# Optimization experiments

Measured on AMD Instinct MI355X. Metric: run time of the kernel, lower is better.

Reference implementation:

```python
import jax, jax.numpy as jnp
import numpy as np

NH = 16  # num_attention_heads
DH = 64  # attention_head_size
HID = NH * DH
TYPE_VOCAB = 2


def setup_inputs() -> dict:
    key = jax.random.key(0)
    ks = jax.random.split(key, 10)
    B, S = 4, 2048
    s = 0.02
    return {
        "hidden_states": jax.random.normal(ks[0], (B, S, HID), jnp.float32),
        "attention_mask": jnp.zeros((B, 1, 1, S), jnp.float32),
        "seg_ids": jax.random.randint(ks[1], (B, S), 0, TYPE_VOCAB),
        "Wq": jax.random.normal(ks[2], (HID, HID), jnp.float32) * s,
        "bq": jnp.zeros((HID,), jnp.float32),
        "Wk": jax.random.normal(ks[3], (HID, HID), jnp.float32) * s,  # key has NO bias (F.linear with weight only)
        "Wv": jax.random.normal(ks[4], (HID, HID), jnp.float32) * s,
        "bv": jnp.zeros((HID,), jnp.float32),
        "seg_table": jax.random.normal(ks[5], (TYPE_VOCAB, HID), jnp.float32) * s,
        "b_q_s": jnp.zeros((1, NH, 1, DH), jnp.float32),
    }


def reference(hidden_states, attention_mask, seg_ids, Wq, bq, Wk, Wv, bv, seg_table, b_q_s):
    B, S, H = hidden_states.shape
    # QKV projections (key projection has no bias, matching F.linear(x, key.weight))
    q = hidden_states @ Wq.T + bq
    k = hidden_states @ Wk.T
    v = hidden_states @ Wv.T + bv
    # [B, NH, S, DH]
    q = q.reshape(B, S, NH, DH).transpose(0, 2, 1, 3)
    k = k.reshape(B, S, NH, DH).transpose(0, 2, 1, 3)
    v = v.reshape(B, S, NH, DH).transpose(0, 2, 1, 3)
    scale = 1.0 / np.sqrt(DH).astype(np.float32)
    scores = jnp.einsum('bhid,bhjd->bhij', q * scale, k)
    # segment-embedding bias: seg_rep [B, S, NH, DH]
    seg_rep = seg_table[seg_ids].reshape(B, S, NH, DH)
    qs = jnp.einsum('bhid,bjhd->bhij', q + b_q_s, seg_rep)
    scores = scores + qs + attention_mask
    probs = jax.nn.softmax(scores, axis=-1)  # dropout: eval mode (identity)
    ctx = jnp.einsum('bhij,bhjd->bihd', probs, v).reshape(B, S, H)
    return ctx
```

## Files before the change

### kernel.cpp

```cpp
#include <hip/hip_runtime.h>
#include <cstdint>
#include <cmath>

#define RLN2 1.44269504088896340736f

typedef __attribute__((ext_vector_type(8))) short short8;
typedef __attribute__((ext_vector_type(4))) short short4v;
typedef __attribute__((ext_vector_type(4))) float f32x4;
typedef __attribute__((ext_vector_type(16))) float f32x16;
typedef __attribute__((ext_vector_type(4))) unsigned int uint4v;

__device__ __forceinline__ unsigned short f2bf(float f) {
  unsigned int u = __float_as_uint(f);
  u += 0x7fffu + ((u >> 16) & 1u);
  return (unsigned short)(u >> 16);
}

__device__ __forceinline__ unsigned int cvt_pk_bf16(float lo, float hi) {
  unsigned int r;
  asm("v_cvt_pk_bf16_f32 %0, %1, %2" : "=v"(r) : "v"(lo), "v"(hi));
  return r;
}

__device__ __forceinline__ float fast_exp2(float x) {
#if __has_builtin(__builtin_amdgcn_exp2f)
  return __builtin_amdgcn_exp2f(x);
#else
  return exp2f(x);
#endif
}

__device__ __forceinline__ void gload16(const void* g, void* l) {
  __builtin_amdgcn_global_load_lds(
      (const __attribute__((address_space(1))) unsigned int*)g,
      (__attribute__((address_space(3))) unsigned int*)l,
      16, 0, 0);
}


__global__ void __launch_bounds__(256) k_cvt_hs(const float* __restrict__ src,
                                                unsigned short* __restrict__ dst) {
  size_t i = (size_t)blockIdx.x * 256 + threadIdx.x;
  const float4* s = (const float4*)src + i * 2;
  float4 a = s[0], b = s[1];
  short8 o;
  o[0] = (short)f2bf(a.x); o[1] = (short)f2bf(a.y); o[2] = (short)f2bf(a.z); o[3] = (short)f2bf(a.w);
  o[4] = (short)f2bf(b.x); o[5] = (short)f2bf(b.y); o[6] = (short)f2bf(b.z); o[7] = (short)f2bf(b.w);
  ((short8*)dst)[i] = o;
}

__global__ void __launch_bounds__(256) k_cvt_w(const float* __restrict__ Wq,
                                               const float* __restrict__ Wk,
                                               const float* __restrict__ Wv,
                                               unsigned short* __restrict__ dst) {
  size_t i = (size_t)blockIdx.x * 256 + threadIdx.x;
  int e = (int)(i * 8);
  int n = e >> 10, c = e & 1023;
  const float* row = (n < 1024) ? (Wq + (size_t)n * 1024)
                   : (n < 2048) ? (Wk + (size_t)(n - 1024) * 1024)
                                : (Wv + (size_t)(n - 2048) * 1024);
  const float4* s = (const float4*)(row + c);
  float4 a = s[0], b = s[1];
  short8 o;
  o[0] = (short)f2bf(a.x); o[1] = (short)f2bf(a.y); o[2] = (short)f2bf(a.z); o[3] = (short)f2bf(a.w);
  o[4] = (short)f2bf(b.x); o[5] = (short)f2bf(b.y); o[6] = (short)f2bf(b.z); o[7] = (short)f2bf(b.w);
  ((short8*)dst)[i] = o;
}

__global__ void __launch_bounds__(256) k_seg(const int* __restrict__ seg_ids,
                                             const float* __restrict__ seg_table,
                                             const float* __restrict__ mask,
                                             unsigned short* __restrict__ Kaug,
                                             float* __restrict__ mask2) {
  size_t i = (size_t)blockIdx.x * 256 + threadIdx.x;
  int e = (int)(i * 8);
  int jl = e >> 10;
  int r  = e & 1023;
  if (r == 0) mask2[jl] = mask[jl] * RLN2;
  int sid = seg_ids[jl];
  const float4* s = (const float4*)(seg_table + (size_t)sid * 1024 + r);
  float4 a = s[0], b = s[1];
  short8 o;
  o[0] = (short)f2bf(a.x); o[1] = (short)f2bf(a.y); o[2] = (short)f2bf(a.z); o[3] = (short)f2bf(a.w);
  o[4] = (short)f2bf(b.x); o[5] = (short)f2bf(b.y); o[6] = (short)f2bf(b.z); o[7] = (short)f2bf(b.w);
  int b_ = jl >> 11, j = jl & 2047;
  int h = r >> 6, d = r & 63;
  size_t off = ((size_t)(b_ * 16 + h) * 2048 + j) * 128 + 64 + d;
  *(short8*)(Kaug + off) = o;
}

__global__ void __launch_bounds__(256) k_gemm(const unsigned short* __restrict__ A,
                                              const unsigned short* __restrict__ Bw,
                                              const float* __restrict__ bq,
                                              const float* __restrict__ bv,
                                              const float* __restrict__ bqs,
                                              unsigned short* __restrict__ Qaug,
                                              unsigned short* __restrict__ Kaug,
                                              unsigned short* __restrict__ Vt) {
  __shared__ unsigned short As[128 * 32];
  __shared__ unsigned short Bs[128 * 32];
  int n0 = blockIdx.x * 128;
  int m0 = blockIdx.y * 128;
  int tid = threadIdx.x;
  int w = tid >> 6, lane = tid & 63;
  int wr = (w >> 1) * 64, wc = (w & 1) * 64;
  int rA = lane & 15;
  int kg = (lane >> 4) * 16;
  f32x4 acc[4][4] = {};
  const char* Ab = (const char*)A;
  const char* Bb = (const char*)Bw;

  for (int kt = 0; kt < 32; ++kt) {
    int kb0 = kt * 64;
#pragma unroll
    for (int c = 0; c < 2; ++c) {
      int chunk = w * 2 + c;
      int y = chunk * 1024 + lane * 16;
      int row = y >> 6, colb = y & 63;
      gload16(Ab + (size_t)(m0 + row) * 2048 + kb0 + colb, (char*)As + chunk * 1024);
      gload16(Bb + (size_t)(n0 + row) * 2048 + kb0 + colb, (char*)Bs + chunk * 1024);
    }
    __syncthreads();
    short8 af[4], bfr[4];
#pragma unroll
    for (int m = 0; m < 4; ++m)
      af[m] = *(const short8*)((const char*)As + (wr + m * 16 + rA) * 64 + kg);
#pragma unroll
    for (int n = 0; n < 4; ++n)
      bfr[n] = *(const short8*)((const char*)Bs + (wc + n * 16 + rA) * 64 + kg);
#pragma unroll
    for (int m = 0; m < 4; ++m)
#pragma unroll
      for (int n = 0; n < 4; ++n)
        acc[m][n] = __builtin_amdgcn_mfma_f32_16x16x32_bf16(af[m], bfr[n], acc[m][n], 0, 0, 0);
    __syncthreads();
  }

  int seg = n0 >> 10;
  int colbase = n0 & 1023;
  int g = lane >> 4;
#pragma unroll
  for (int n = 0; n < 4; ++n) {
    int o = colbase + wc + n * 16 + (lane & 15);
    int h = o >> 6, d = o & 63;
    float bias = 0.f, bqsv = 0.f;
    if (seg == 0) { bias = bq[o]; bqsv = bqs[o]; }
    else if (seg == 2) { bias = bv[o]; }
#pragma unroll
    for (int m = 0; m < 4; ++m) {
      if (seg == 2) {
        int i = m0 + wr + m * 16 + g * 4;
        int b_ = i >> 11, sdx = i & 2047;
        int bh = b_ * 16 + h;
        int pos = (sdx & ~63) + 32 * ((m >> 1) & 1) + 16 * (m & 1) + 8 * (g & 1) + 4 * ((g >> 1) & 1);
        short4v pv;
#pragma unroll
        for (int r = 0; r < 4; ++r)
          pv[r] = (short)f2bf(acc[m][n][r] + bias);
        *(short4v*)(Vt + (size_t)bh * 131072 + (size_t)d * 2048 + pos) = pv;
      } else {
#pragma unroll
        for (int r = 0; r < 4; ++r) {
          int i = m0 + wr + m * 16 + g * 4 + r;
          int b_ = i >> 11, sdx = i & 2047;
          float val = acc[m][n][r];
          size_t tok = (size_t)(b_ * 16 + h) * 2048 + sdx;
          if (seg == 0) {
            float qv = val + bias;
            Qaug[tok * 128 + d]      = f2bf(qv * (0.125f * RLN2));
            Qaug[tok * 128 + 64 + d] = f2bf((qv + bqsv) * RLN2);
          } else {
            Kaug[tok * 128 + d] = f2bf(val);
          }
        }
      }
    }
  }
}

__global__ void __launch_bounds__(512, 4) k_attn(const unsigned short* __restrict__ Qaug,
                                                 const unsigned short* __restrict__ Kaug,
                                                 const unsigned short* __restrict__ Vt,
                                                 const float* __restrict__ mask2,
                                                 float* __restrict__ out) {
  __shared__ char smem[49152];
  char* Ksb = smem;
  char* Vsb = smem + 32768;

  int qt = blockIdx.x, h = blockIdx.y, b_ = blockIdx.z;
  int bh = b_ * 16 + h;
  int i0 = qt * 256;
  int tid = threadIdx.x, w = tid >> 6, lane = tid & 63;
  int q = lane & 31, hi = lane >> 5;
  int swzq = (q & 7) << 4;
  const char* Qg = (const char*)Qaug + (size_t)bh * 2048 * 256;
  const char* Kg = (const char*)Kaug + (size_t)bh * 2048 * 256;
  const char* Vg = (const char*)Vt + (size_t)bh * 64 * 4096;
  const float* maskb = mask2 + (size_t)b_ * 2048;

  int foff[8];
#pragma unroll
  for (int ds = 0; ds < 8; ++ds)
    foff[ds] = (ds * 32 + hi * 16) ^ swzq;

  int kst_row = lane >> 4, kst_x = (lane & 15) * 16;
  int vst_dv = lane >> 3;
  int vst_x = ((lane & 7) * 16) ^ ((vst_dv & 7) << 4);

#pragma unroll
  for (int c = 0; c < 2; ++c) {
    int ck = w * 2 + c;
    int krow = ck * 4 + kst_row;
    gload16(Kg + (size_t)krow * 256 + (kst_x ^ ((krow & 7) << 4)), Ksb + ck * 1024);
  }
  {
    int dv = w * 8 + vst_dv;
    gload16(Vg + (size_t)dv * 4096 + vst_x, Vsb + w * 1024);
  }

  short8 qf[8];
  {
    const char* qrow = Qg + (size_t)(i0 + w * 32 + q) * 256 + hi * 16;
#pragma unroll
    for (int ds = 0; ds < 8; ++ds)
      qf[ds] = *(const short8*)(qrow + ds * 32);
  }
  __syncthreads();

  float m_run = -1e30f, l_run = 0.f;
  f32x16 accO[2] = {};

  for (int t = 0; t < 32; ++t) {
    int cur = t & 1, nxt = cur ^ 1;
    int j0 = t * 64;
    if (t < 31) {
      int jn = j0 + 64;
      char* kd = Ksb + nxt * 16384;
      char* vd = Vsb + nxt * 8192;
#pragma unroll
      for (int c = 0; c < 2; ++c) {
        int ck = w * 2 + c;
        int krow = ck * 4 + kst_row;
        gload16(Kg + (size_t)(jn + krow) * 256 + (kst_x ^ ((krow & 7) << 4)), kd + ck * 1024);
      }
      {
        int dv = w * 8 + vst_dv;
        gload16(Vg + (size_t)dv * 4096 + jn * 2 + vst_x, vd + w * 1024);
      }
    }
    const char* kq = Ksb + cur * 16384 + q * 256;
    const char* vq = Vsb + cur * 8192 + q * 128;

    f32x16 s0 = {}, s1 = {};
    __builtin_amdgcn_s_setprio(1);
#pragma unroll
    for (int ds = 0; ds < 8; ++ds) {
      short8 kf0 = *(const short8*)(kq + foff[ds]);
      short8 kf1 = *(const short8*)(kq + foff[ds] + 8192);
      s0 = __builtin_amdgcn_mfma_f32_32x32x16_bf16(kf0, qf[ds], s0, 0, 0, 0);
      s1 = __builtin_amdgcn_mfma_f32_32x32x16_bf16(kf1, qf[ds], s1, 0, 0, 0);
    }
    __builtin_amdgcn_s_setprio(0);

#pragma unroll
    for (int c = 0; c < 4; ++c) {
      f32x4 mv0 = *(const f32x4*)(maskb + j0 + 8 * c + 4 * hi);
      f32x4 mv1 = *(const f32x4*)(maskb + j0 + 32 + 8 * c + 4 * hi);
#pragma unroll
      for (int r = 0; r < 4; ++r) {
        s0[4 * c + r] += mv0[r];
        s1[4 * c + r] += mv1[r];
      }
    }

    {
      f32x16 mx;
#pragma unroll
      for (int i = 0; i < 16; ++i) mx[i] = fmaxf(s0[i], s1[i]);
#pragma unroll
      for (int i = 0; i < 8; ++i) mx[i] = fmaxf(mx[i], mx[i + 8]);
#pragma unroll
      for (int i = 0; i < 4; ++i) mx[i] = fmaxf(mx[i], mx[i + 4]);
      float tm = fmaxf(fmaxf(mx[0], mx[1]), fmaxf(mx[2], mx[3]));
      tm = fmaxf(tm, __shfl_xor(tm, 32));

      if (__any(tm > m_run + 8.0f)) {
        float mn = fmaxf(m_run, tm);
        float alpha = fast_exp2(m_run - mn);
        m_run = mn;
        l_run *= alpha;
#pragma unroll
        for (int i = 0; i < 16; ++i) { accO[0][i] *= alpha; accO[1][i] *= alpha; }
      }
    }
    {
      f32x16 es;
#pragma unroll
      for (int i = 0; i < 16; ++i) {
        float e0 = fast_exp2(s0[i] - m_run);
        float e1 = fast_exp2(s1[i] - m_run);
        s0[i] = e0; s1[i] = e1;
        es[i] = e0 + e1;
      }
#pragma unroll
      for (int i = 0; i < 8; ++i) es[i] += es[i + 8];
#pragma unroll
      for (int i = 0; i < 4; ++i) es[i] += es[i + 4];
      float ps = (es[0] + es[1]) + (es[2] + es[3]);
      ps += __shfl_xor(ps, 32);
      l_run += ps;
    }

    uint4v pk[4];
#pragma unroll
    for (int ks = 0; ks < 4; ++ks) {
      int o = 8 * (ks & 1);
      const f32x16& sv = (ks < 2) ? s0 : s1;
      pk[ks][0] = cvt_pk_bf16(sv[o + 0], sv[o + 1]);
      pk[ks][1] = cvt_pk_bf16(sv[o + 2], sv[o + 3]);
      pk[ks][2] = cvt_pk_bf16(sv[o + 4], sv[o + 5]);
      pk[ks][3] = cvt_pk_bf16(sv[o + 6], sv[o + 7]);
    }

    __builtin_amdgcn_s_setprio(1);
#pragma unroll
    for (int ks = 0; ks < 4; ++ks) {
      short8 pf = __builtin_bit_cast(short8, pk[ks]);
      short8 vf0 = *(const short8*)(vq + foff[ks]);
      short8 vf1 = *(const short8*)(vq + foff[ks] + 4096);
      accO[0] = __builtin_amdgcn_mfma_f32_32x32x16_bf16(vf0, pf, accO[0], 0, 0, 0);
      accO[1] = __builtin_amdgcn_mfma_f32_32x32x16_bf16(vf1, pf, accO[1], 0, 0, 0);
    }
    __builtin_amdgcn_s_setprio(0);
    __syncthreads();
  }

  float inv = 1.0f / l_run;
  float* orow = out + ((size_t)b_ * 2048 + i0 + w * 32 + q) * 1024 + h * 64;
#pragma unroll
  for (int vh = 0; vh < 2; ++vh) {
#pragma unroll
    for (int c = 0; c < 4; ++c) {
      f32x4 o;
      o[0] = accO[vh][4 * c + 0] * inv;
      o[1] = accO[vh][4 * c + 1] * inv;
      o[2] = accO[vh][4 * c + 2] * inv;
      o[3] = accO[vh][4 * c + 3] * inv;
      *(f32x4*)(orow + vh * 32 + 8 * c + 4 * hi) = o;
    }
  }
}

extern "C" void kernel_launch(void* const* d_in, const int* in_sizes, int n_in,
                              void* d_out, int out_size, void* d_ws, size_t ws_size,
                              hipStream_t stream) {
  (void)in_sizes; (void)n_in; (void)out_size; (void)ws_size;
  const float* hs        = (const float*)d_in[0];
  const float* mask      = (const float*)d_in[1];
  const int*   seg_ids   = (const int*)d_in[2];
  const float* Wq        = (const float*)d_in[3];
  const float* bq        = (const float*)d_in[4];
  const float* Wk        = (const float*)d_in[5];
  const float* Wv        = (const float*)d_in[6];
  const float* bv        = (const float*)d_in[7];
  const float* seg_table = (const float*)d_in[8];
  const float* bqs       = (const float*)d_in[9];
  float* out = (float*)d_out;
  char* ws = (char*)d_ws;

  unsigned short* hsb  = (unsigned short*)(ws + 0);
  unsigned short* Wcat = (unsigned short*)(ws + 16777216);
  unsigned short* Qaug = (unsigned short*)(ws + 23068672);
  unsigned short* Kaug = (unsigned short*)(ws + 56623104);
  unsigned short* Vt   = (unsigned short*)(ws + 90177536);
  float*          mask2 = (float*)(ws + 0);

  k_cvt_hs<<<dim3(4096), dim3(256), 0, stream>>>(hs, hsb);
  k_cvt_w<<<dim3(1536), dim3(256), 0, stream>>>(Wq, Wk, Wv, Wcat);
  k_gemm<<<dim3(24, 64), dim3(256), 0, stream>>>(hsb, Wcat, bq, bv, bqs, Qaug, Kaug, Vt);
  k_seg<<<dim3(4096), dim3(256), 0, stream>>>(seg_ids, seg_table, mask, Kaug, mask2);
  k_attn<<<dim3(8, 16, 4), dim3(512), 0, stream>>>(Qaug, Kaug, Vt, mask2, out);
}
```

Before: 267.8 us.

## Split KV tile into two 32-key halves for softmax/MFMA overlap

The 64-key inner tile is now processed as two 32-key halves, each with its own online-softmax update followed by its PV MFMAs. The QK MFMAs for the second half can overlap the softmax of the first half, and the mask loads are hoisted ahead of the MFMAs. In exchange, the max/rescale check and the rescale of accO run twice per tile, and the QK MFMA chains become serial dependency chains of 8 instead of two interleaved chains.

```diff
diff --git a/kernel.cpp b/kernel.cpp
--- a/kernel.cpp
+++ b/kernel.cpp
@@ -251,39 +251,40 @@
     const char* kq = Ksb + cur * 16384 + q * 256;
     const char* vq = Vsb + cur * 8192 + q * 128;
 
+    f32x4 mv0[4], mv1[4];
+#pragma unroll
+    for (int c = 0; c < 4; ++c) {
+      mv0[c] = *(const f32x4*)(maskb + j0 + 8 * c + 4 * hi);
+      mv1[c] = *(const f32x4*)(maskb + j0 + 32 + 8 * c + 4 * hi);
+    }
+
     f32x16 s0 = {}, s1 = {};
     __builtin_amdgcn_s_setprio(1);
 #pragma unroll
     for (int ds = 0; ds < 8; ++ds) {
       short8 kf0 = *(const short8*)(kq + foff[ds]);
+      s0 = __builtin_amdgcn_mfma_f32_32x32x16_bf16(kf0, qf[ds], s0, 0, 0, 0);
+    }
+#pragma unroll
+    for (int ds = 0; ds < 8; ++ds) {
       short8 kf1 = *(const short8*)(kq + foff[ds] + 8192);
-      s0 = __builtin_amdgcn_mfma_f32_32x32x16_bf16(kf0, qf[ds], s0, 0, 0, 0);
       s1 = __builtin_amdgcn_mfma_f32_32x32x16_bf16(kf1, qf[ds], s1, 0, 0, 0);
     }
     __builtin_amdgcn_s_setprio(0);
 
-#pragma unroll
-    for (int c = 0; c < 4; ++c) {
-      f32x4 mv0 = *(const f32x4*)(maskb + j0 + 8 * c + 4 * hi);
-      f32x4 mv1 = *(const f32x4*)(maskb + j0 + 32 + 8 * c + 4 * hi);
-#pragma unroll
-      for (int r = 0; r < 4; ++r) {
-        s0[4 * c + r] += mv0[r];
-        s1[4 * c + r] += mv1[r];
-      }
-    }
-
+    uint4v pkA[2];
     {
-      f32x16 mx;
-#pragma unroll
-      for (int i = 0; i < 16; ++i) mx[i] = fmaxf(s0[i], s1[i]);
-#pragma unroll
-      for (int i = 0; i < 8; ++i) mx[i] = fmaxf(mx[i], mx[i + 8]);
-#pragma unroll
-      for (int i = 0; i < 4; ++i) mx[i] = fmaxf(mx[i], mx[i + 4]);
+#pragma unroll
+      for (int c = 0; c < 4; ++c)
+#pragma unroll
+        for (int r = 0; r < 4; ++r)
+          s0[4 * c + r] += mv0[c][r];
+      f32x4 mx;
+#pragma unroll
+      for (int i = 0; i < 4; ++i)
+        mx[i] = fmaxf(fmaxf(s0[i], s0[i + 4]), fmaxf(s0[i + 8], s0[i + 12]));
       float tm = fmaxf(fmaxf(mx[0], mx[1]), fmaxf(mx[2], mx[3]));
       tm = fmaxf(tm, __shfl_xor(tm, 32));
-
       if (__any(tm > m_run + 8.0f)) {
         float mn = fmaxf(m_run, tm);
         float alpha = fast_exp2(m_run - mn);
@@ -292,16 +293,9 @@
 #pragma unroll
         for (int i = 0; i < 16; ++i) { accO[0][i] *= alpha; accO[1][i] *= alpha; }
       }
-    }
-    {
       f32x16 es;
 #pragma unroll
-      for (int i = 0; i < 16; ++i) {
-        float e0 = fast_exp2(s0[i] - m_run);
-        float e1 = fast_exp2(s1[i] - m_run);
-        s0[i] = e0; s1[i] = e1;
-        es[i] = e0 + e1;
-      }
+      for (int i = 0; i < 16; ++i) { es[i] = fast_exp2(s0[i] - m_run); s0[i] = es[i]; }
 #pragma unroll
       for (int i = 0; i < 8; ++i) es[i] += es[i + 8];
 #pragma unroll
@@ -309,25 +303,74 @@
       float ps = (es[0] + es[1]) + (es[2] + es[3]);
       ps += __shfl_xor(ps, 32);
       l_run += ps;
-    }
-
-    uint4v pk[4];
-#pragma unroll
-    for (int ks = 0; ks < 4; ++ks) {
-      int o = 8 * (ks & 1);
-      const f32x16& sv = (ks < 2) ? s0 : s1;
-      pk[ks][0] = cvt_pk_bf16(sv[o + 0], sv[o + 1]);
-      pk[ks][1] = cvt_pk_bf16(sv[o + 2], sv[o + 3]);
-      pk[ks][2] = cvt_pk_bf16(sv[o + 4], sv[o + 5]);
-      pk[ks][3] = cvt_pk_bf16(sv[o + 6], sv[o + 7]);
+      pkA[0][0] = cvt_pk_bf16(s0[0], s0[1]);
+      pkA[0][1] = cvt_pk_bf16(s0[2], s0[3]);
+      pkA[0][2] = cvt_pk_bf16(s0[4], s0[5]);
+      pkA[0][3] = cvt_pk_bf16(s0[6], s0[7]);
+      pkA[1][0] = cvt_pk_bf16(s0[8], s0[9]);
+      pkA[1][1] = cvt_pk_bf16(s0[10], s0[11]);
+      pkA[1][2] = cvt_pk_bf16(s0[12], s0[13]);
+      pkA[1][3] = cvt_pk_bf16(s0[14], s0[15]);
     }
 
     __builtin_amdgcn_s_setprio(1);
 #pragma unroll
-    for (int ks = 0; ks < 4; ++ks) {
-      short8 pf = __builtin_bit_cast(short8, pk[ks]);
+    for (int ks = 0; ks < 2; ++ks) {
+      short8 pf = __builtin_bit_cast(short8, pkA[ks]);
       short8 vf0 = *(const short8*)(vq + foff[ks]);
       short8 vf1 = *(const short8*)(vq + foff[ks] + 4096);
+      accO[0] = __builtin_amdgcn_mfma_f32_32x32x16_bf16(vf0, pf, accO[0], 0, 0, 0);
+      accO[1] = __builtin_amdgcn_mfma_f32_32x32x16_bf16(vf1, pf, accO[1], 0, 0, 0);
+    }
+    __builtin_amdgcn_s_setprio(0);
+
+    uint4v pkB[2];
+    {
+#pragma unroll
+      for (int c = 0; c < 4; ++c)
+#pragma unroll
+        for (int r = 0; r < 4; ++r)
+          s1[4 * c + r] += mv1[c][r];
+      f32x4 mx;
+#pragma unroll
+      for (int i = 0; i < 4; ++i)
+        mx[i] = fmaxf(fmaxf(s1[i], s1[i + 4]), fmaxf(s1[i + 8], s1[i + 12]));
+      float tm = fmaxf(fmaxf(mx[0], mx[1]), fmaxf(mx[2], mx[3]));
+      tm = fmaxf(tm, __shfl_xor(tm, 32));
+      if (__any(tm > m_run + 8.0f)) {
+        float mn = fmaxf(m_run, tm);
+        float alpha = fast_exp2(m_run - mn);
+        m_run = mn;
+        l_run *= alpha;
+#pragma unroll
+        for (int i = 0; i < 16; ++i) { accO[0][i] *= alpha; accO[1][i] *= alpha; }
+      }
+      f32x16 es;
+#pragma unroll
+      for (int i = 0; i < 16; ++i) { es[i] = fast_exp2(s1[i] - m_run); s1[i] = es[i]; }
+#pragma unroll
+      for (int i = 0; i < 8; ++i) es[i] += es[i + 8];
+#pragma unroll
+      for (int i = 0; i < 4; ++i) es[i] += es[i + 4];
+      float ps = (es[0] + es[1]) + (es[2] + es[3]);
+      ps += __shfl_xor(ps, 32);
+      l_run += ps;
+      pkB[0][0] = cvt_pk_bf16(s1[0], s1[1]);
+      pkB[0][1] = cvt_pk_bf16(s1[2], s1[3]);
+      pkB[0][2] = cvt_pk_bf16(s1[4], s1[5]);
+      pkB[0][3] = cvt_pk_bf16(s1[6], s1[7]);
+      pkB[1][0] = cvt_pk_bf16(s1[8], s1[9]);
+      pkB[1][1] = cvt_pk_bf16(s1[10], s1[11]);
+      pkB[1][2] = cvt_pk_bf16(s1[12], s1[13]);
+      pkB[1][3] = cvt_pk_bf16(s1[14], s1[15]);
+    }
+
+    __builtin_amdgcn_s_setprio(1);
+#pragma unroll
+    for (int ks = 0; ks < 2; ++ks) {
+      short8 pf = __builtin_bit_cast(short8, pkB[ks]);
+      short8 vf0 = *(const short8*)(vq + foff[ks + 2]);
+      short8 vf1 = *(const short8*)(vq + foff[ks + 2] + 4096);
       accO[0] = __builtin_amdgcn_mfma_f32_32x32x16_bf16(vf0, pf, accO[0], 0, 0, 0);
       accO[1] = __builtin_amdgcn_mfma_f32_32x32x16_bf16(vf1, pf, accO[1], 0, 0, 0);
     }
```

Result: slower. 962.2 us (+259.4%).

## Fuse prep kernels into one launch and vectorize Q/K GEMM epilogue stores

Applied to the files above, without the earlier changes.

Merges the three conversion and segment-embedding kernels into a single k_prep launch and drops the mask2 buffer, folding the log2(e) mask scaling into an fma inside the attention kernel. For Q and K tiles the GEMM swaps its MFMA operands so each lane holds four consecutive output columns. This lets the epilogue write packed 8-byte bf16 stores through v_cvt_pk_bf16 instead of scattered 2-byte stores. The aim is to cut launch overhead and uncoalesced epilogue writes, at the cost of a seg-dependent branch in the MFMA loop.

```diff
diff --git a/kernel.cpp b/kernel.cpp
--- a/kernel.cpp
+++ b/kernel.cpp
@@ -9,6 +9,7 @@
 typedef __attribute__((ext_vector_type(4))) float f32x4;
 typedef __attribute__((ext_vector_type(16))) float f32x16;
 typedef __attribute__((ext_vector_type(4))) unsigned int uint4v;
+typedef __attribute__((ext_vector_type(2))) unsigned int uint2v;
 
 __device__ __forceinline__ unsigned short f2bf(float f) {
   unsigned int u = __float_as_uint(f);
@@ -37,56 +38,53 @@
       16, 0, 0);
 }
 
-
-__global__ void __launch_bounds__(256) k_cvt_hs(const float* __restrict__ src,
-                                                unsigned short* __restrict__ dst) {
-  size_t i = (size_t)blockIdx.x * 256 + threadIdx.x;
-  const float4* s = (const float4*)src + i * 2;
-  float4 a = s[0], b = s[1];
-  short8 o;
-  o[0] = (short)f2bf(a.x); o[1] = (short)f2bf(a.y); o[2] = (short)f2bf(a.z); o[3] = (short)f2bf(a.w);
-  o[4] = (short)f2bf(b.x); o[5] = (short)f2bf(b.y); o[6] = (short)f2bf(b.z); o[7] = (short)f2bf(b.w);
-  ((short8*)dst)[i] = o;
-}
-
-__global__ void __launch_bounds__(256) k_cvt_w(const float* __restrict__ Wq,
-                                               const float* __restrict__ Wk,
-                                               const float* __restrict__ Wv,
-                                               unsigned short* __restrict__ dst) {
-  size_t i = (size_t)blockIdx.x * 256 + threadIdx.x;
-  int e = (int)(i * 8);
-  int n = e >> 10, c = e & 1023;
-  const float* row = (n < 1024) ? (Wq + (size_t)n * 1024)
-                   : (n < 2048) ? (Wk + (size_t)(n - 1024) * 1024)
-                                : (Wv + (size_t)(n - 2048) * 1024);
-  const float4* s = (const float4*)(row + c);
-  float4 a = s[0], b = s[1];
-  short8 o;
-  o[0] = (short)f2bf(a.x); o[1] = (short)f2bf(a.y); o[2] = (short)f2bf(a.z); o[3] = (short)f2bf(a.w);
-  o[4] = (short)f2bf(b.x); o[5] = (short)f2bf(b.y); o[6] = (short)f2bf(b.z); o[7] = (short)f2bf(b.w);
-  ((short8*)dst)[i] = o;
-}
-
-__global__ void __launch_bounds__(256) k_seg(const int* __restrict__ seg_ids,
-                                             const float* __restrict__ seg_table,
-                                             const float* __restrict__ mask,
-                                             unsigned short* __restrict__ Kaug,
-                                             float* __restrict__ mask2) {
-  size_t i = (size_t)blockIdx.x * 256 + threadIdx.x;
-  int e = (int)(i * 8);
-  int jl = e >> 10;
-  int r  = e & 1023;
-  if (r == 0) mask2[jl] = mask[jl] * RLN2;
-  int sid = seg_ids[jl];
-  const float4* s = (const float4*)(seg_table + (size_t)sid * 1024 + r);
-  float4 a = s[0], b = s[1];
-  short8 o;
-  o[0] = (short)f2bf(a.x); o[1] = (short)f2bf(a.y); o[2] = (short)f2bf(a.z); o[3] = (short)f2bf(a.w);
-  o[4] = (short)f2bf(b.x); o[5] = (short)f2bf(b.y); o[6] = (short)f2bf(b.z); o[7] = (short)f2bf(b.w);
-  int b_ = jl >> 11, j = jl & 2047;
-  int h = r >> 6, d = r & 63;
-  size_t off = ((size_t)(b_ * 16 + h) * 2048 + j) * 128 + 64 + d;
-  *(short8*)(Kaug + off) = o;
+__global__ void __launch_bounds__(256) k_prep(const float* __restrict__ hs,
+                                              const float* __restrict__ Wq,
+                                              const float* __restrict__ Wk,
+                                              const float* __restrict__ Wv,
+                                              const int* __restrict__ seg_ids,
+                                              const float* __restrict__ seg_table,
+                                              unsigned short* __restrict__ hsb,
+                                              unsigned short* __restrict__ Wcat,
+                                              unsigned short* __restrict__ Kaug) {
+  int blk = blockIdx.x;
+  if (blk < 4096) {
+    size_t i = (size_t)blk * 256 + threadIdx.x;
+    const float4* s = (const float4*)hs + i * 2;
+    float4 a = s[0], b = s[1];
+    short8 o;
+    o[0] = (short)f2bf(a.x); o[1] = (short)f2bf(a.y); o[2] = (short)f2bf(a.z); o[3] = (short)f2bf(a.w);
+    o[4] = (short)f2bf(b.x); o[5] = (short)f2bf(b.y); o[6] = (short)f2bf(b.z); o[7] = (short)f2bf(b.w);
+    ((short8*)hsb)[i] = o;
+  } else if (blk < 5632) {
+    size_t i = (size_t)(blk - 4096) * 256 + threadIdx.x;
+    int e = (int)(i * 8);
+    int n = e >> 10, c = e & 1023;
+    const float* row = (n < 1024) ? (Wq + (size_t)n * 1024)
+                     : (n < 2048) ? (Wk + (size_t)(n - 1024) * 1024)
+                                  : (Wv + (size_t)(n - 2048) * 1024);
+    const float4* s = (const float4*)(row + c);
+    float4 a = s[0], b = s[1];
+    short8 o;
+    o[0] = (short)f2bf(a.x); o[1] = (short)f2bf(a.y); o[2] = (short)f2bf(a.z); o[3] = (short)f2bf(a.w);
+    o[4] = (short)f2bf(b.x); o[5] = (short)f2bf(b.y); o[6] = (short)f2bf(b.z); o[7] = (short)f2bf(b.w);
+    ((short8*)Wcat)[i] = o;
+  } else {
+    size_t i = (size_t)(blk - 5632) * 256 + threadIdx.x;
+    int e = (int)(i * 8);
+    int jl = e >> 10;
+    int r  = e & 1023;
+    int sid = seg_ids[jl];
+    const float4* s = (const float4*)(seg_table + (size_t)sid * 1024 + r);
+    float4 a = s[0], b = s[1];
+    short8 o;
+    o[0] = (short)f2bf(a.x); o[1] = (short)f2bf(a.y); o[2] = (short)f2bf(a.z); o[3] = (short)f2bf(a.w);
+    o[4] = (short)f2bf(b.x); o[5] = (short)f2bf(b.y); o[6] = (short)f2bf(b.z); o[7] = (short)f2bf(b.w);
+    int b_ = jl >> 11, j = jl & 2047;
+    int h = r >> 6, d = r & 63;
+    size_t off = ((size_t)(b_ * 16 + h) * 2048 + j) * 128 + 64 + d;
+    *(short8*)(Kaug + off) = o;
+  }
 }
 
 __global__ void __launch_bounds__(256) k_gemm(const unsigned short* __restrict__ A,
@@ -106,6 +104,7 @@
   int wr = (w >> 1) * 64, wc = (w & 1) * 64;
   int rA = lane & 15;
   int kg = (lane >> 4) * 16;
+  int seg = n0 >> 10;
   f32x4 acc[4][4] = {};
   const char* Ab = (const char*)A;
   const char* Bb = (const char*)Bw;
@@ -128,27 +127,32 @@
 #pragma unroll
     for (int n = 0; n < 4; ++n)
       bfr[n] = *(const short8*)((const char*)Bs + (wc + n * 16 + rA) * 64 + kg);
-#pragma unroll
-    for (int m = 0; m < 4; ++m)
-#pragma unroll
-      for (int n = 0; n < 4; ++n)
-        acc[m][n] = __builtin_amdgcn_mfma_f32_16x16x32_bf16(af[m], bfr[n], acc[m][n], 0, 0, 0);
+    if (seg == 2) {
+#pragma unroll
+      for (int m = 0; m < 4; ++m)
+#pragma unroll
+        for (int n = 0; n < 4; ++n)
+          acc[m][n] = __builtin_amdgcn_mfma_f32_16x16x32_bf16(af[m], bfr[n], acc[m][n], 0, 0, 0);
+    } else {
+#pragma unroll
+      for (int m = 0; m < 4; ++m)
+#pragma unroll
+        for (int n = 0; n < 4; ++n)
+          acc[m][n] = __builtin_amdgcn_mfma_f32_16x16x32_bf16(bfr[n], af[m], acc[m][n], 0, 0, 0);
+    }
     __syncthreads();
   }
 
-  int seg = n0 >> 10;
   int colbase = n0 & 1023;
   int g = lane >> 4;
-#pragma unroll
-  for (int n = 0; n < 4; ++n) {
-    int o = colbase + wc + n * 16 + (lane & 15);
-    int h = o >> 6, d = o & 63;
-    float bias = 0.f, bqsv = 0.f;
-    if (seg == 0) { bias = bq[o]; bqsv = bqs[o]; }
-    else if (seg == 2) { bias = bv[o]; }
-#pragma unroll
-    for (int m = 0; m < 4; ++m) {
-      if (seg == 2) {
+  if (seg == 2) {
+#pragma unroll
+    for (int n = 0; n < 4; ++n) {
+      int o = colbase + wc + n * 16 + (lane & 15);
+      int h = o >> 6, d = o & 63;
+      float bias = bv[o];
+#pragma unroll
+      for (int m = 0; m < 4; ++m) {
         int i = m0 + wr + m * 16 + g * 4;
         int b_ = i >> 11, sdx = i & 2047;
         int bh = b_ * 16 + h;
@@ -158,20 +162,38 @@
         for (int r = 0; r < 4; ++r)
           pv[r] = (short)f2bf(acc[m][n][r] + bias);
         *(short4v*)(Vt + (size_t)bh * 131072 + (size_t)d * 2048 + pos) = pv;
-      } else {
-#pragma unroll
-        for (int r = 0; r < 4; ++r) {
-          int i = m0 + wr + m * 16 + g * 4 + r;
-          int b_ = i >> 11, sdx = i & 2047;
-          float val = acc[m][n][r];
-          size_t tok = (size_t)(b_ * 16 + h) * 2048 + sdx;
-          if (seg == 0) {
-            float qv = val + bias;
-            Qaug[tok * 128 + d]      = f2bf(qv * (0.125f * RLN2));
-            Qaug[tok * 128 + 64 + d] = f2bf((qv + bqsv) * RLN2);
-          } else {
-            Kaug[tok * 128 + d] = f2bf(val);
-          }
+      }
+    }
+  } else {
+    int tok16 = lane & 15, g4 = g * 4;
+#pragma unroll
+    for (int m = 0; m < 4; ++m) {
+      int i = m0 + wr + m * 16 + tok16;
+      int b_ = i >> 11, sdx = i & 2047;
+#pragma unroll
+      for (int n = 0; n < 4; ++n) {
+        int o0 = colbase + wc + n * 16 + g4;
+        int h = o0 >> 6, d0 = o0 & 63;
+        size_t tok = (size_t)(b_ * 16 + h) * 2048 + sdx;
+        if (seg == 0) {
+          f32x4 bqv = *(const f32x4*)(bq + o0);
+          f32x4 bqs4 = *(const f32x4*)(bqs + o0);
+          float qv0 = acc[m][n][0] + bqv[0], qv1 = acc[m][n][1] + bqv[1];
+          float qv2 = acc[m][n][2] + bqv[2], qv3 = acc[m][n][3] + bqv[3];
+          const float sc = 0.125f * RLN2;
+          uint2v p1;
+          p1[0] = cvt_pk_bf16(qv0 * sc, qv1 * sc);
+          p1[1] = cvt_pk_bf16(qv2 * sc, qv3 * sc);
+          *(uint2v*)(Qaug + tok * 128 + d0) = p1;
+          uint2v p2;
+          p2[0] = cvt_pk_bf16((qv0 + bqs4[0]) * RLN2, (qv1 + bqs4[1]) * RLN2);
+          p2[1] = cvt_pk_bf16((qv2 + bqs4[2]) * RLN2, (qv3 + bqs4[3]) * RLN2);
+          *(uint2v*)(Qaug + tok * 128 + 64 + d0) = p2;
+        } else {
+          uint2v p1;
+          p1[0] = cvt_pk_bf16(acc[m][n][0], acc[m][n][1]);
+          p1[1] = cvt_pk_bf16(acc[m][n][2], acc[m][n][3]);
+          *(uint2v*)(Kaug + tok * 128 + d0) = p1;
         }
       }
     }
@@ -181,7 +203,7 @@
 __global__ void __launch_bounds__(512, 4) k_attn(const unsigned short* __restrict__ Qaug,
                                                  const unsigned short* __restrict__ Kaug,
                                                  const unsigned short* __restrict__ Vt,
-                                                 const float* __restrict__ mask2,
+                                                 const float* __restrict__ mask,
                                                  float* __restrict__ out) {
   __shared__ char smem[49152];
   char* Ksb = smem;
@@ -196,7 +218,7 @@
   const char* Qg = (const char*)Qaug + (size_t)bh * 2048 * 256;
   const char* Kg = (const char*)Kaug + (size_t)bh * 2048 * 256;
   const char* Vg = (const char*)Vt + (size_t)bh * 64 * 4096;
-  const float* maskb = mask2 + (size_t)b_ * 2048;
+  const float* maskb = mask + (size_t)b_ * 2048;
 
   int foff[8];
 #pragma unroll
@@ -268,8 +290,8 @@
       f32x4 mv1 = *(const f32x4*)(maskb + j0 + 32 + 8 * c + 4 * hi);
 #pragma unroll
       for (int r = 0; r < 4; ++r) {
-        s0[4 * c + r] += mv0[r];
-        s1[4 * c + r] += mv1[r];
+        s0[4 * c + r] = fmaf(mv0[r], RLN2, s0[4 * c + r]);
+        s1[4 * c + r] = fmaf(mv1[r], RLN2, s1[4 * c + r]);
       }
     }
 
@@ -373,11 +395,9 @@
   unsigned short* Qaug = (unsigned short*)(ws + 23068672);
   unsigned short* Kaug = (unsigned short*)(ws + 56623104);
   unsigned short* Vt   = (unsigned short*)(ws + 90177536);
-  float*          mask2 = (float*)(ws + 0);
-
-  k_cvt_hs<<<dim3(4096), dim3(256), 0, stream>>>(hs, hsb);
-  k_cvt_w<<<dim3(1536), dim3(256), 0, stream>>>(Wq, Wk, Wv, Wcat);
+
+  k_prep<<<dim3(9728), dim3(256), 0, stream>>>(hs, Wq, Wk, Wv, seg_ids, seg_table,
+                                               hsb, Wcat, Kaug);
   k_gemm<<<dim3(24, 64), dim3(256), 0, stream>>>(hsb, Wcat, bq, bv, bqs, Qaug, Kaug, Vt);
-  k_seg<<<dim3(4096), dim3(256), 0, stream>>>(seg_ids, seg_table, mask, Kaug, mask2);
-  k_attn<<<dim3(8, 16, 4), dim3(512), 0, stream>>>(Qaug, Kaug, Vt, mask2, out);
-}
+  k_attn<<<dim3(8, 16, 4), dim3(512), 0, stream>>>(Qaug, Kaug, Vt, mask, out);
+}
```

After: 253.6 us, median of 2. 5.3% less time.
